# Performance work log

Measured on AMD Instinct MI355X. Metric: run time of the kernel, lower is better.

## Reference

```python
import jax, jax.numpy as jnp
import numpy as np

B, T, S, DM, H, HID = 4, 1024, 1024, 1024, 16, 4096
DEPTH = DM // H


def setup_inputs() -> dict:
    key = jax.random.key(0)
    ks = jax.random.split(key, 32)
    n = lambda k, shape, scale=1.0: jax.random.normal(k, shape, dtype=jnp.float32) * scale
    w_scale = 1.0 / np.sqrt(DM)
    inp = {
        "x": n(ks[0], (B, T, DM)),
        "enc_out": n(ks[1], (B, S, DM)),
        # causal mask: 1 where attention is forbidden (TF convention mask*-1e9)
        "look_ahead_mask": jnp.broadcast_to(
            jnp.triu(jnp.ones((T, T), jnp.float32), k=1), (B, 1, T, T)),
        "padding_mask": jnp.zeros((B, 1, 1, S), jnp.float32),
    }
    # self-attention MHA params
    names = ["wq1", "wk1", "wv1", "wo1", "wq2", "wk2", "wv2", "wo2"]
    for i, nm in enumerate(names):
        inp[nm] = n(ks[2 + i], (DM, DM), w_scale)
        inp["b" + nm[1:]] = jnp.zeros((DM,), jnp.float32)
    # FFN
    inp["wh"] = n(ks[10], (DM, HID), w_scale)
    inp["bh"] = jnp.zeros((HID,), jnp.float32)
    inp["wout"] = n(ks[11], (HID, DM), 1.0 / np.sqrt(HID))
    inp["bout"] = jnp.zeros((DM,), jnp.float32)
    for i in (1, 2, 3):
        inp[f"g{i}"] = jnp.ones((DM,), jnp.float32)
        inp[f"be{i}"] = jnp.zeros((DM,), jnp.float32)
    return inp


def _layer_norm(x, gamma, beta, eps=1e-6):
    mean = jnp.mean(x, axis=-1, keepdims=True)
    var = jnp.mean(jnp.square(x - mean), axis=-1, keepdims=True)
    return gamma * (x - mean) * jax.lax.rsqrt(var + eps) + beta


def _mha(q_in, k_in, v_in, mask, wq, bq, wk, bk, wv, bv, wo, bo):
    b = q_in.shape[0]
    split = lambda t: t.reshape(b, -1, H, DEPTH).transpose(0, 2, 1, 3)  # [b,h,s,d]
    Q = split(q_in @ wq + bq)
    K = split(k_in @ wk + bk)
    V = split(v_in @ wv + bv)
    scores = jnp.einsum("bhqd,bhkd->bhqk", Q, K) / jnp.sqrt(jnp.float32(DEPTH))
    scores = scores + mask * (-1e9)
    w = jax.nn.softmax(scores, axis=-1)
    out = jnp.einsum("bhqk,bhkd->bhqd", w, V)
    out = out.transpose(0, 2, 1, 3).reshape(b, -1, DM)
    return out @ wo + bo


def reference(x, enc_out, look_ahead_mask, padding_mask,
              wq1, bq1, wk1, bk1, wv1, bv1, wo1, bo1,
              wq2, bq2, wk2, bk2, wv2, bv2, wo2, bo2,
              wh, bh, wout, bout, g1, be1, g2, be2, g3, be3):
    # self-attention + residual + LN (dropout identity at inference)
    a1 = _mha(x, x, x, look_ahead_mask, wq1, bq1, wk1, bk1, wv1, bv1, wo1, bo1)
    h1 = _layer_norm(a1 + x, g1, be1)
    # cross-attention + residual + LN
    a2 = _mha(h1, enc_out, enc_out, padding_mask,
              wq2, bq2, wk2, bk2, wv2, bv2, wo2, bo2)
    h2 = _layer_norm(a2 + h1, g2, be2)
    # FFN + residual + LN
    f = jax.nn.relu(h2 @ wh + bh) @ wout + bout
    return _layer_norm(f + h2, g3, be3)
```

## Files before the change

kernel.cpp:

```cpp
#include <hip/hip_runtime.h>
#include <hip/hip_bf16.h>

typedef __bf16 bf16;
typedef __bf16 bf16x4 __attribute__((ext_vector_type(4)));
typedef __bf16 bf16x8 __attribute__((ext_vector_type(8)));
typedef float floatx4 __attribute__((ext_vector_type(4)));

#define MFMA16(a, b, c) __builtin_amdgcn_mfma_f32_16x16x32_bf16(a, b, c, 0, 0, 0)

#define BB   4
#define TT   1024
#define SS   1024
#define DMOD 1024
#define NH   16
#define DH   64
#define HID  4096
#define MTOT (BB * TT)

__device__ __forceinline__ float loadf(const bf16* p)  { return (float)*p; }
__device__ __forceinline__ float loadf(const float* p) { return *p; }

__device__ __forceinline__ void gll16(const bf16* g, bf16* l) {
    __builtin_amdgcn_global_load_lds(
        (const __attribute__((address_space(1))) void*)g,
        (__attribute__((address_space(3))) void*)l, 16, 0, 0);
}

__device__ __forceinline__ void xcd_swizzle2d(int& bx, int& by) {
    const int gx  = gridDim.x;
    const int nwg = gx * gridDim.y;
    const int lin = blockIdx.y * gx + blockIdx.x;
    const int q   = nwg >> 3;
    const int swz = (lin & 7) * q + (lin >> 3);
    bx = swz % gx;
    by = swz / gx;
}

struct TBatch { const float* src[8]; bf16* dst[8]; };

__global__ __launch_bounds__(256)
void transpose_sq_kernel(TBatch tb)
{
    __shared__ float t[64][65];
    const float* W = tb.src[blockIdx.z];
    bf16* WT = tb.dst[blockIdx.z];
    const int k0 = blockIdx.y * 64, n0 = blockIdx.x * 64;
    const int tid = threadIdx.x;
    const int r = tid >> 4, c = (tid & 15) * 4;
    #pragma unroll
    for (int i = 0; i < 4; ++i) {
        float4 v = *(const float4*)(W + (size_t)(k0 + i * 16 + r) * DMOD + n0 + c);
        t[i * 16 + r][c + 0] = v.x; t[i * 16 + r][c + 1] = v.y;
        t[i * 16 + r][c + 2] = v.z; t[i * 16 + r][c + 3] = v.w;
    }
    __syncthreads();
    #pragma unroll
    for (int i = 0; i < 4; ++i) {
        int n = i * 16 + r;
        bf16x4 o;
        #pragma unroll
        for (int j = 0; j < 4; ++j) o[j] = (bf16)t[c + j][n];
        *(bf16x4*)(WT + (size_t)(n0 + n) * DMOD + k0 + c) = o;
    }
}

__global__ __launch_bounds__(256)
void transpose_kernel(const float* __restrict__ W, bf16* __restrict__ WT, int K, int N)
{
    __shared__ float t[64][65];
    const int k0 = blockIdx.y * 64, n0 = blockIdx.x * 64;
    const int tid = threadIdx.x;
    const int r = tid >> 4, c = (tid & 15) * 4;
    #pragma unroll
    for (int i = 0; i < 4; ++i) {
        float4 v = *(const float4*)(W + (size_t)(k0 + i * 16 + r) * N + n0 + c);
        t[i * 16 + r][c + 0] = v.x; t[i * 16 + r][c + 1] = v.y;
        t[i * 16 + r][c + 2] = v.z; t[i * 16 + r][c + 3] = v.w;
    }
    __syncthreads();
    #pragma unroll
    for (int i = 0; i < 4; ++i) {
        int n = i * 16 + r;
        bf16x4 o;
        #pragma unroll
        for (int j = 0; j < 4; ++j) o[j] = (bf16)t[c + j][n];
        *(bf16x4*)(WT + (size_t)(n0 + n) * K + k0 + c) = o;
    }
}

__global__ __launch_bounds__(256)
void vtrans_kernel(const bf16* __restrict__ in, int ldi, bf16* __restrict__ out)
{
    __shared__ bf16 t[64][72];
    const int r0 = blockIdx.y * 64;
    const int c0 = blockIdx.x * 64;
    const int tid = threadIdx.x;
    const int rr = tid >> 3;
    const int c8 = (tid & 7) * 8;
    #pragma unroll
    for (int i = 0; i < 2; ++i) {
        int row = i * 32 + rr;
        bf16x8 v = *(const bf16x8*)(in + (size_t)(r0 + row) * ldi + c0 + c8);
        *(bf16x8*)(&t[row][c8]) = v;
    }
    __syncthreads();
    #pragma unroll
    for (int i = 0; i < 2; ++i) {
        int col = i * 32 + rr;
        bf16x8 v;
        #pragma unroll
        for (int j = 0; j < 8; ++j) v[j] = t[c8 + j][col];
        *(bf16x8*)(out + (size_t)(c0 + col) * MTOT + r0 + c8) = v;
    }
}

__global__ __launch_bounds__(256)
void cvt_kernel(const float* __restrict__ in, bf16* __restrict__ out, int n4)
{
    int i = blockIdx.x * 256 + threadIdx.x;
    if (i < n4) {
        float4 v = ((const float4*)in)[i];
        bf16x4 o = { (bf16)v.x, (bf16)v.y, (bf16)v.z, (bf16)v.w };
        ((bf16x4*)out)[i] = o;
    }
}

__global__ __launch_bounds__(256)
void bias_concat_kernel(const float* bq1, const float* bk1, const float* bv1,
                        const float* bk2, const float* bv2, float* __restrict__ biasc)
{
    int i = blockIdx.x * 256 + threadIdx.x;
    float v;
    if      (i < 1024) v = bq1[i];
    else if (i < 2048) v = bk1[i - 1024];
    else if (i < 3072) v = bv1[i - 2048];
    else if (i < 4096) v = bk2[i - 3072];
    else               v = bv2[i - 4096];
    if (i < 5120) biasc[i] = v;
}

template <int EPI, typename TR>
__global__ __launch_bounds__(256, 4)
void gemm128k32_kernel(const bf16* __restrict__ A, int lda, const bf16* __restrict__ B,
                       const float* __restrict__ bias, const TR* __restrict__ resid,
                       bf16* __restrict__ out, int M, int N, int K)
{
    __shared__ bf16 Al[2][128 * 32];
    __shared__ bf16 Bl[2][128 * 32];

    const int tid  = threadIdx.x;
    const int wave = tid >> 6;
    const int lane = tid & 63;
    const int l16  = lane & 15;
    const int quad = lane >> 4;
    int bx, by;
    xcd_swizzle2d(bx, by);
    const int bm   = by * 128;
    const int bn   = bx * 128;
    const int wm   = (wave >> 1) * 64;
    const int wn   = (wave & 1) * 64;
    const int lrow = lane >> 2;
    const int scol = ((lane & 3) ^ ((lane >> 3) & 3)) * 8;

    floatx4 acc[4][4] = {};
    const int ntk = K / 32;

    auto STAGE = [&](int kt, int buf) {
        const int k0 = kt * 32;
        #pragma unroll
        for (int i = 0; i < 2; ++i) {
            int r0 = (wave * 2 + i) * 16;
            gll16(A + (size_t)(bm + r0 + lrow) * lda + k0 + scol, &Al[buf][r0 * 32]);
            gll16(B + (size_t)(bn + r0 + lrow) * K   + k0 + scol, &Bl[buf][r0 * 32]);
        }
    };

    auto COMPUTE = [&](int buf) {
        bf16x8 af[4], bg[4];
        const int xo = ((quad ^ ((l16 >> 1) & 3))) * 8;
        #pragma unroll
        for (int mt = 0; mt < 4; ++mt)
            af[mt] = *(const bf16x8*)(&Al[buf][(wm + mt * 16 + l16) * 32 + xo]);
        #pragma unroll
        for (int nt = 0; nt < 4; ++nt)
            bg[nt] = *(const bf16x8*)(&Bl[buf][(wn + nt * 16 + l16) * 32 + xo]);
        #pragma unroll
        for (int mt = 0; mt < 4; ++mt)
            #pragma unroll
            for (int nt = 0; nt < 4; ++nt)
                acc[mt][nt] = MFMA16(af[mt], bg[nt], acc[mt][nt]);
    };

    STAGE(0, 0);
    asm volatile("s_waitcnt vmcnt(0)" ::: "memory");
    __builtin_amdgcn_s_barrier();

    int cur = 0;
    for (int t = 0; t < ntk - 1; ++t) {
        STAGE(t + 1, cur ^ 1);
        COMPUTE(cur);
        asm volatile("s_waitcnt vmcnt(0) lgkmcnt(0)" ::: "memory");
        __builtin_amdgcn_s_barrier();
        cur ^= 1;
    }
    COMPUTE(cur);

    #pragma unroll
    for (int mt = 0; mt < 4; ++mt) {
        int row0 = bm + wm + mt * 16 + quad * 4;
        #pragma unroll
        for (int nt = 0; nt < 4; ++nt) {
            int col = bn + wn + nt * 16 + l16;
            float bv = bias[col];
            #pragma unroll
            for (int r = 0; r < 4; ++r) {
                float v = acc[mt][nt][r] + bv;
                size_t idx = (size_t)(row0 + r) * N + col;
                if (EPI == 1) v = fmaxf(v, 0.0f);
                if (EPI == 2) v += loadf(resid + idx);
                out[idx] = (bf16)v;
            }
        }
    }
}

template <int EPI, typename TR>
__global__ __launch_bounds__(256, 4)
void gemm6464_kernel(const bf16* __restrict__ A, int lda, const bf16* __restrict__ B,
                     const float* __restrict__ bias, const TR* __restrict__ resid,
                     bf16* __restrict__ out, int M, int N, int K)
{
    __shared__ bf16 Al[2][64 * 64];
    __shared__ bf16 Bl[2][64 * 64];

    const int tid  = threadIdx.x;
    const int wave = tid >> 6;
    const int lane = tid & 63;
    const int l16  = lane & 15;
    const int quad = lane >> 4;
    int bx, by;
    xcd_swizzle2d(bx, by);
    const int bm   = by * 64;
    const int bn   = bx * 64;
    const int wm   = (wave >> 1) * 32;
    const int wn   = (wave & 1) * 32;
    const int lrow = lane >> 3;
    const int scol = ((lane & 7) ^ lrow) * 8;

    floatx4 acc[2][2] = {};
    const int ntk = K / 64;

    auto STAGE = [&](int kt, int buf) {
        const int k0 = kt * 64;
        #pragma unroll
        for (int i = 0; i < 2; ++i) {
            int r0 = wave * 16 + i * 8;
            gll16(A + (size_t)(bm + r0 + lrow) * lda + k0 + scol, &Al[buf][r0 * 64]);
            gll16(B + (size_t)(bn + r0 + lrow) * K   + k0 + scol, &Bl[buf][r0 * 64]);
        }
    };

    auto COMPUTE = [&](int buf) {
        #pragma unroll
        for (int ks = 0; ks < 2; ++ks) {
            bf16x8 af[2], bg[2];
            const int xo = ((ks * 4 + quad) ^ (l16 & 7)) * 8;
            #pragma unroll
            for (int mt = 0; mt < 2; ++mt)
                af[mt] = *(const bf16x8*)(&Al[buf][(wm + mt * 16 + l16) * 64 + xo]);
            #pragma unroll
            for (int nt = 0; nt < 2; ++nt)
                bg[nt] = *(const bf16x8*)(&Bl[buf][(wn + nt * 16 + l16) * 64 + xo]);
            #pragma unroll
            for (int mt = 0; mt < 2; ++mt)
                #pragma unroll
                for (int nt = 0; nt < 2; ++nt)
                    acc[mt][nt] = MFMA16(af[mt], bg[nt], acc[mt][nt]);
        }
    };

    STAGE(0, 0);
    asm volatile("s_waitcnt vmcnt(0)" ::: "memory");
    __builtin_amdgcn_s_barrier();

    int cur = 0;
    for (int t = 0; t < ntk - 1; ++t) {
        STAGE(t + 1, cur ^ 1);
        COMPUTE(cur);
        asm volatile("s_waitcnt vmcnt(0) lgkmcnt(0)" ::: "memory");
        __builtin_amdgcn_s_barrier();
        cur ^= 1;
    }
    COMPUTE(cur);

    #pragma unroll
    for (int mt = 0; mt < 2; ++mt) {
        int row0 = bm + wm + mt * 16 + quad * 4;
        #pragma unroll
        for (int nt = 0; nt < 2; ++nt) {
            int col = bn + wn + nt * 16 + l16;
            float bv = bias[col];
            #pragma unroll
            for (int r = 0; r < 4; ++r) {
                float v = acc[mt][nt][r] + bv;
                size_t idx = (size_t)(row0 + r) * N + col;
                if (EPI == 1) v = fmaxf(v, 0.0f);
                if (EPI == 2) v += loadf(resid + idx);
                out[idx] = (bf16)v;
            }
        }
    }
}

template <int CAUSAL>
__global__ __launch_bounds__(256, 3)
void attn_kernel(const bf16* __restrict__ Q, int ldq, const bf16* __restrict__ K, int ldk,
                 const bf16* __restrict__ Vt, bf16* __restrict__ O, int ldo)
{
    __shared__ bf16 Kl[2][64 * 64];
    __shared__ bf16 Vl[2][64 * 64];
    __shared__ bf16 Pl[4 * 16 * 72];

    const int tid  = threadIdx.x;
    const int wave = tid >> 6;
    const int lane = tid & 63;
    const int l16  = lane & 15;
    const int quad = lane >> 4;
    int bx, byy, bz;
    {
        const int lin = (blockIdx.z * 16 + blockIdx.y) * 16 + blockIdx.x;
        const int swz = (lin & 7) * 128 + (lin >> 3);
        bx  = swz & 15;
        byy = (swz >> 4) & 15;
        bz  = swz >> 8;
    }
    const int qb   = CAUSAL ? (15 - bx) : bx;
    const int h    = byy;
    const int b    = bz;

    const int qrow0 = b * TT + qb * 64 + wave * 16;
    const int colh  = h * DH;
    const int lr8   = lane >> 3;
    const int lc8s  = ((lane & 7) ^ lr8) * 8;

    bf16x8 qa[2];
    #pragma unroll
    for (int c = 0; c < 2; ++c)
        qa[c] = *(const bf16x8*)(Q + (size_t)(qrow0 + l16) * ldq + colh + c * 32 + quad * 8);

    floatx4 o[5] = {};
    const float C = 0.125f * 1.4426950408889634f;
    bf16x8 onesf;
    {
        bf16 ov = (bf16)((l16 == 0) ? 1.0f : 0.0f);
        #pragma unroll
        for (int j = 0; j < 8; ++j) onesf[j] = ov;
    }

    const int ntiles = CAUSAL ? qb + 1 : (SS / 64);
    bf16* pw = Pl + wave * (16 * 72);

    auto STAGE = [&](int t, int buf) {
        const int kv0 = t * 64;
        #pragma unroll
        for (int i = 0; i < 2; ++i) {
            int r0 = wave * 16 + i * 8;
            gll16(K  + (size_t)(b * SS + kv0 + r0 + lr8) * ldk + colh + lc8s, &Kl[buf][r0 * 64]);
            gll16(Vt + (size_t)(colh + r0 + lr8) * MTOT + b * SS + kv0 + lc8s, &Vl[buf][r0 * 64]);
        }
    };

    auto COMPUTE = [&](int t, int buf) {
        const int xo0 = (quad ^ (l16 & 7)) * 8;
        const int xo1 = ((4 + quad) ^ (l16 & 7)) * 8;

        floatx4 s[4];
        #pragma unroll
        for (int nt = 0; nt < 4; ++nt) {
            bf16x8 kb0 = *(const bf16x8*)(&Kl[buf][(nt * 16 + l16) * 64 + xo0]);
            bf16x8 kb1 = *(const bf16x8*)(&Kl[buf][(nt * 16 + l16) * 64 + xo1]);
            floatx4 z = {};
            z = MFMA16(qa[0], kb0, z);
            z = MFMA16(qa[1], kb1, z);
            s[nt] = z;
        }

        const bool dm = CAUSAL && (t == qb);
        #pragma unroll
        for (int nt = 0; nt < 4; ++nt)
            #pragma unroll
            for (int r = 0; r < 4; ++r) {
                float sv = s[nt][r] * C;
                if (dm) {
                    int qg  = wave * 16 + quad * 4 + r;
                    int kvg = nt * 16 + l16;
                    if (kvg > qg) sv = -1e30f;
                }
                float pv = exp2f(sv);
                pw[(quad * 4 + r) * 72 + nt * 16 + l16] = (bf16)pv;
            }

        bf16x8 pa0 = *(const bf16x8*)(pw + l16 * 72 + quad * 8);
        bf16x8 pa1 = *(const bf16x8*)(pw + l16 * 72 + 32 + quad * 8);
        #pragma unroll
        for (int dt = 0; dt < 4; ++dt) {
            bf16x8 vb0 = *(const bf16x8*)(&Vl[buf][(dt * 16 + l16) * 64 + xo0]);
            bf16x8 vb1 = *(const bf16x8*)(&Vl[buf][(dt * 16 + l16) * 64 + xo1]);
            o[dt] = MFMA16(pa0, vb0, o[dt]);
            o[dt] = MFMA16(pa1, vb1, o[dt]);
        }
        o[4] = MFMA16(pa0, onesf, o[4]);
        o[4] = MFMA16(pa1, onesf, o[4]);
    };

    STAGE(0, 0);
    asm volatile("s_waitcnt vmcnt(0)" ::: "memory");
    __builtin_amdgcn_s_barrier();

    int cur = 0;
    for (int t = 0; t < ntiles - 1; ++t) {
        STAGE(t + 1, cur ^ 1);
        COMPUTE(t, cur);
        asm volatile("s_waitcnt vmcnt(0) lgkmcnt(0)" ::: "memory");
        __builtin_amdgcn_s_barrier();
        cur ^= 1;
    }
    COMPUTE(ntiles - 1, cur);

    #pragma unroll
    for (int r = 0; r < 4; ++r) {
        float lr  = __shfl(o[4][r], (lane & 48));
        float inv = __builtin_amdgcn_rcpf(lr);
        #pragma unroll
        for (int dt = 0; dt < 4; ++dt) {
            float ov = o[dt][r] * inv;
            size_t idx = (size_t)(qrow0 + quad * 4 + r) * ldo + colh + dt * 16 + l16;
            O[idx] = (bf16)ov;
        }
    }
}

template <typename TO>
__global__ __launch_bounds__(256)
void ln_kernel(const bf16* __restrict__ in, const float* __restrict__ g,
               const float* __restrict__ be, TO* __restrict__ out)
{
    const int row = blockIdx.x;
    const int tid = threadIdx.x;
    bf16x4 xv = *(const bf16x4*)(in + (size_t)row * DMOD + tid * 4);
    float x0 = (float)xv[0], x1 = (float)xv[1], x2 = (float)xv[2], x3 = (float)xv[3];

    float s = x0 + x1 + x2 + x3;
    #pragma unroll
    for (int off = 32; off >= 1; off >>= 1) s += __shfl_xor(s, off);
    __shared__ float red1[4];
    __shared__ float red2[4];
    const int wave = tid >> 6;
    if ((tid & 63) == 0) red1[wave] = s;
    __syncthreads();
    float mean = (red1[0] + red1[1] + red1[2] + red1[3]) * (1.0f / DMOD);

    float d0 = x0 - mean, d1 = x1 - mean, d2 = x2 - mean, d3 = x3 - mean;
    float sq = d0 * d0 + d1 * d1 + d2 * d2 + d3 * d3;
    #pragma unroll
    for (int off = 32; off >= 1; off >>= 1) sq += __shfl_xor(sq, off);
    if ((tid & 63) == 0) red2[wave] = sq;
    __syncthreads();
    float var = (red2[0] + red2[1] + red2[2] + red2[3]) * (1.0f / DMOD);
    float rs = rsqrtf(var + 1e-6f);

    int c = tid * 4;
    size_t o0 = (size_t)row * DMOD + c;
    out[o0 + 0] = (TO)(g[c + 0] * d0 * rs + be[c + 0]);
    out[o0 + 1] = (TO)(g[c + 1] * d1 * rs + be[c + 1]);
    out[o0 + 2] = (TO)(g[c + 2] * d2 * rs + be[c + 2]);
    out[o0 + 3] = (TO)(g[c + 3] * d3 * rs + be[c + 3]);
}

extern "C" void kernel_launch(void* const* d_in, const int* in_sizes, int n_in,
                              void* d_out, int out_size, void* d_ws, size_t ws_size,
                              hipStream_t stream)
{
    const float* x   = (const float*)d_in[0];
    const float* enc = (const float*)d_in[1];
    const float* wq1 = (const float*)d_in[4];  const float* bq1 = (const float*)d_in[5];
    const float* wk1 = (const float*)d_in[6];  const float* bk1 = (const float*)d_in[7];
    const float* wv1 = (const float*)d_in[8];  const float* bv1 = (const float*)d_in[9];
    const float* wo1 = (const float*)d_in[10]; const float* bo1 = (const float*)d_in[11];
    const float* wq2 = (const float*)d_in[12]; const float* bq2 = (const float*)d_in[13];
    const float* wk2 = (const float*)d_in[14]; const float* bk2 = (const float*)d_in[15];
    const float* wv2 = (const float*)d_in[16]; const float* bv2 = (const float*)d_in[17];
    const float* wo2 = (const float*)d_in[18]; const float* bo2 = (const float*)d_in[19];
    const float* wh  = (const float*)d_in[20]; const float* bh  = (const float*)d_in[21];
    const float* wou = (const float*)d_in[22]; const float* bou = (const float*)d_in[23];
    const float* g1  = (const float*)d_in[24]; const float* be1 = (const float*)d_in[25];
    const float* g2  = (const float*)d_in[26]; const float* be2 = (const float*)d_in[27];
    const float* g3  = (const float*)d_in[28]; const float* be3 = (const float*)d_in[29];

    const int M = MTOT;
    const size_t MB = 1u << 20;
    dim3 blk(256);

    char* ws = (char*)d_ws;
    bf16*  WT    = (bf16*)(ws);
    float* biasc = (float*)(ws + 8 * MB);
    bf16*  xb    = (bf16*)(ws + 9 * MB);
    bf16*  h1    = (bf16*)(ws + 9 * MB);
    bf16*  tmpb3 = (bf16*)(ws + 9 * MB);
    bf16*  encb  = (bf16*)(ws + 17 * MB);
    bf16*  Vt2   = (bf16*)(ws + 17 * MB);
    bf16*  ffn   = (bf16*)(ws + 17 * MB);
    bf16*  qkv   = (bf16*)(ws + 25 * MB);
    bf16*  kvb   = qkv + (size_t)M * 1024;
    bf16*  tmpb2 = qkv + (size_t)M * 1024;
    bf16*  Vt1   = (bf16*)(ws + 49 * MB);
    bf16*  tmpb1 = (bf16*)(ws + 49 * MB);
    bf16*  h2    = (bf16*)(ws + 49 * MB);

    dim3 gThi(HID / 64, DMOD / 64);
    dim3 gTout(DMOD / 64, HID / 64);
    dim3 gVt(DMOD / 64, M / 64);
    dim3 gQKV(3072 / 128, M / 128);
    dim3 gKV(2048 / 128, M / 128);
    dim3 gH(HID / 128, M / 128);
    dim3 gN6464(DMOD / 64, M / 64);
    dim3 gA(TT / 64, NH, BB);
    const size_t W1M = (size_t)1024 * 1024;

    cvt_kernel<<<dim3(M * DMOD / 4 / 256), blk, 0, stream>>>(x, xb, M * DMOD / 4);
    cvt_kernel<<<dim3(M * DMOD / 4 / 256), blk, 0, stream>>>(enc, encb, M * DMOD / 4);
    bias_concat_kernel<<<dim3(20), blk, 0, stream>>>(bq1, bk1, bv1, bk2, bv2, biasc);

    {
        TBatch tb;
        tb.src[0] = wq1; tb.dst[0] = WT + 0 * W1M;
        tb.src[1] = wk1; tb.dst[1] = WT + 1 * W1M;
        tb.src[2] = wv1; tb.dst[2] = WT + 2 * W1M;
        tb.src[3] = wo1; tb.dst[3] = WT + 3 * W1M;
        tb.src[4] = tb.src[5] = tb.src[6] = tb.src[7] = wq1;
        tb.dst[4] = tb.dst[5] = tb.dst[6] = tb.dst[7] = WT;
        dim3 g4(16, 16, 4);
        transpose_sq_kernel<<<g4, blk, 0, stream>>>(tb);
    }

    gemm128k32_kernel<0, bf16><<<gQKV, blk, 0, stream>>>(xb, 1024, WT, biasc,
                                                         (const bf16*)nullptr, qkv, M, 3072, 1024);
    vtrans_kernel<<<gVt, blk, 0, stream>>>(qkv + 2048, 3072, Vt1);
    attn_kernel<1><<<gA, blk, 0, stream>>>(qkv, 3072, qkv + 1024, 3072, Vt1, qkv, 3072);
    gemm6464_kernel<2, float><<<gN6464, blk, 0, stream>>>(qkv, 3072, WT + 3 * W1M, bo1, x,
                                                          tmpb1, M, 1024, 1024);
    ln_kernel<bf16><<<dim3(M), blk, 0, stream>>>(tmpb1, g1, be1, h1);

    {
        TBatch tb;
        tb.src[0] = wq2; tb.dst[0] = WT + 0 * W1M;
        tb.src[1] = wk2; tb.dst[1] = WT + 1 * W1M;
        tb.src[2] = wv2; tb.dst[2] = WT + 2 * W1M;
        tb.src[3] = wo2; tb.dst[3] = WT + 3 * W1M;
        tb.src[4] = tb.src[5] = tb.src[6] = tb.src[7] = wq2;
        tb.dst[4] = tb.dst[5] = tb.dst[6] = tb.dst[7] = WT;
        dim3 g4(16, 16, 4);
        transpose_sq_kernel<<<g4, blk, 0, stream>>>(tb);
    }

    gemm6464_kernel<0, bf16><<<gN6464, blk, 0, stream>>>(h1, 1024, WT, bq2, (const bf16*)nullptr,
                                                         qkv, M, 1024, 1024);
    gemm128k32_kernel<0, bf16><<<gKV, blk, 0, stream>>>(encb, 1024, WT + 1 * W1M, biasc + 3072,
                                                        (const bf16*)nullptr, kvb, M, 2048, 1024);
    vtrans_kernel<<<gVt, blk, 0, stream>>>(kvb + 1024, 2048, Vt2);
    attn_kernel<0><<<gA, blk, 0, stream>>>(qkv, 1024, kvb, 2048, Vt2, qkv, 1024);
    gemm6464_kernel<2, bf16><<<gN6464, blk, 0, stream>>>(qkv, 1024, WT + 3 * W1M, bo2, h1,
                                                         tmpb2, M, 1024, 1024);
    ln_kernel<bf16><<<dim3(M), blk, 0, stream>>>(tmpb2, g2, be2, h2);

    transpose_kernel<<<gThi, blk, 0, stream>>>(wh, WT, DMOD, HID);
    gemm128k32_kernel<1, bf16><<<gH, blk, 0, stream>>>(h2, 1024, WT, bh, (const bf16*)nullptr,
                                                       ffn, M, HID, 1024);
    transpose_kernel<<<gTout, blk, 0, stream>>>(wou, WT, HID, DMOD);
    gemm6464_kernel<2, bf16><<<gN6464, blk, 0, stream>>>(ffn, 4096, WT, bou, h2,
                                                         tmpb3, M, 1024, 4096);
    ln_kernel<float><<<dim3(M), blk, 0, stream>>>(tmpb3, g3, be3, (float*)d_out);
}
```

Baseline: 500.9 us.

## Use 64x128 tiles for QKV/KV GEMMs and split-K FFN2 fused into LayerNorm

Adds a 64x128 tile GEMM with BK=32 for the fused QKV and cross-attention KV projections, which doubles the number of blocks and raises occupancy. Adds a split-K (K/2) 64x64 GEMM for the FFN down-projection. It writes two bf16 partials, which a new LayerNorm kernel sums together with the bias and residual. This spreads the K=4096 GEMM over more blocks, at the cost of extra partial-buffer traffic and bf16 rounding of the partials. The split-K path is taken only when the workspace is at least 66MB.

```diff
diff --git a/kernel.cpp b/kernel.cpp
--- a/kernel.cpp
+++ b/kernel.cpp
@@ -177,7 +177,7 @@
 
     auto COMPUTE = [&](int buf) {
         bf16x8 af[4], bg[4];
-        const int xo = ((quad ^ ((l16 >> 1) & 3))) * 8;
+        const int xo = (quad ^ ((l16 >> 1) & 3)) * 8;
         #pragma unroll
         for (int mt = 0; mt < 4; ++mt)
             af[mt] = *(const bf16x8*)(&Al[buf][(wm + mt * 16 + l16) * 32 + xo]);
@@ -219,6 +219,90 @@
                 if (EPI == 1) v = fmaxf(v, 0.0f);
                 if (EPI == 2) v += loadf(resid + idx);
                 out[idx] = (bf16)v;
+            }
+        }
+    }
+}
+
+__global__ __launch_bounds__(256, 6)
+void gemm64128k32_kernel(const bf16* __restrict__ A, int lda, const bf16* __restrict__ B,
+                         const float* __restrict__ bias, bf16* __restrict__ out,
+                         int M, int N, int K)
+{
+    __shared__ bf16 Al[2][64 * 32];
+    __shared__ bf16 Bl[2][128 * 32];
+
+    const int tid  = threadIdx.x;
+    const int wave = tid >> 6;
+    const int lane = tid & 63;
+    const int l16  = lane & 15;
+    const int quad = lane >> 4;
+    int bx, by;
+    xcd_swizzle2d(bx, by);
+    const int bm   = by * 64;
+    const int bn   = bx * 128;
+    const int wm   = (wave >> 1) * 32;
+    const int wn   = (wave & 1) * 64;
+    const int lrow = lane >> 2;
+    const int scol = ((lane & 3) ^ ((lane >> 3) & 3)) * 8;
+
+    floatx4 acc[2][4] = {};
+    const int ntk = K / 32;
+
+    auto STAGE = [&](int kt, int buf) {
+        const int k0 = kt * 32;
+        {
+            int r0 = wave * 16;
+            gll16(A + (size_t)(bm + r0 + lrow) * lda + k0 + scol, &Al[buf][r0 * 32]);
+        }
+        #pragma unroll
+        for (int i = 0; i < 2; ++i) {
+            int r0 = wave * 32 + i * 16;
+            gll16(B + (size_t)(bn + r0 + lrow) * K + k0 + scol, &Bl[buf][r0 * 32]);
+        }
+    };
+
+    auto COMPUTE = [&](int buf) {
+        bf16x8 af[2], bg[4];
+        const int xo = (quad ^ ((l16 >> 1) & 3)) * 8;
+        #pragma unroll
+        for (int mt = 0; mt < 2; ++mt)
+            af[mt] = *(const bf16x8*)(&Al[buf][(wm + mt * 16 + l16) * 32 + xo]);
+        #pragma unroll
+        for (int nt = 0; nt < 4; ++nt)
+            bg[nt] = *(const bf16x8*)(&Bl[buf][(wn + nt * 16 + l16) * 32 + xo]);
+        #pragma unroll
+        for (int mt = 0; mt < 2; ++mt)
+            #pragma unroll
+            for (int nt = 0; nt < 4; ++nt)
+                acc[mt][nt] = MFMA16(af[mt], bg[nt], acc[mt][nt]);
+    };
+
+    STAGE(0, 0);
+    asm volatile("s_waitcnt vmcnt(0)" ::: "memory");
+    __builtin_amdgcn_s_barrier();
+
+    int cur = 0;
+    for (int t = 0; t < ntk - 1; ++t) {
+        STAGE(t + 1, cur ^ 1);
+        COMPUTE(cur);
+        asm volatile("s_waitcnt vmcnt(0) lgkmcnt(0)" ::: "memory");
+        __builtin_amdgcn_s_barrier();
+        cur ^= 1;
+    }
+    COMPUTE(cur);
+
+    #pragma unroll
+    for (int mt = 0; mt < 2; ++mt) {
+        int row0 = bm + wm + mt * 16 + quad * 4;
+        #pragma unroll
+        for (int nt = 0; nt < 4; ++nt) {
+            int col = bn + wn + nt * 16 + l16;
+            float bv = bias[col];
+            #pragma unroll
+            for (int r = 0; r < 4; ++r) {
+                float v = acc[mt][nt][r] + bv;
+                out[(size_t)(row0 + r) * N + col] = (bf16)v;
             }
         }
     }
@@ -312,6 +396,84 @@
     }
 }
 
+__global__ __launch_bounds__(256, 8)
+void gemm6464k32s_kernel(const bf16* __restrict__ A, int lda, const bf16* __restrict__ B,
+                         bf16* __restrict__ p0, bf16* __restrict__ p1,
+                         int M, int N, int K)
+{
+    __shared__ bf16 Al[2][64 * 32];
+    __shared__ bf16 Bl[2][64 * 32];
+
+    const int tid  = threadIdx.x;
+    const int wave = tid >> 6;
+    const int lane = tid & 63;
+    const int l16  = lane & 15;
+    const int quad = lane >> 4;
+    int bx, by;
+    xcd_swizzle2d(bx, by);
+    const int bm   = by * 64;
+    const int bn   = bx * 64;
+    const int wm   = (wave >> 1) * 32;
+    const int wn   = (wave & 1) * 32;
+    const int lrow = lane >> 2;
+    const int scol = ((lane & 3) ^ ((lane >> 3) & 3)) * 8;
+    const int kh    = K >> 1;
+    const int kbase = blockIdx.z * kh;
+    bf16* outp = blockIdx.z ? p1 : p0;
+
+    floatx4 acc[2][2] = {};
+    const int ntk = kh / 32;
+
+    auto STAGE = [&](int kt, int buf) {
+        const int k0 = kbase + kt * 32;
+        int r0 = wave * 16;
+        gll16(A + (size_t)(bm + r0 + lrow) * lda + k0 + scol, &Al[buf][r0 * 32]);
+        gll16(B + (size_t)(bn + r0 + lrow) * K   + k0 + scol, &Bl[buf][r0 * 32]);
+    };
+
+    auto COMPUTE = [&](int buf) {
+        bf16x8 af[2], bg[2];
+        const int xo = (quad ^ ((l16 >> 1) & 3)) * 8;
+        #pragma unroll
+        for (int mt = 0; mt < 2; ++mt)
+            af[mt] = *(const bf16x8*)(&Al[buf][(wm + mt * 16 + l16) * 32 + xo]);
+        #pragma unroll
+        for (int nt = 0; nt < 2; ++nt)
+            bg[nt] = *(const bf16x8*)(&Bl[buf][(wn + nt * 16 + l16) * 32 + xo]);
+        #pragma unroll
+        for (int mt = 0; mt < 2; ++mt)
+            #pragma unroll
+            for (int nt = 0; nt < 2; ++nt)
+                acc[mt][nt] = MFMA16(af[mt], bg[nt], acc[mt][nt]);
+    };
+
+    STAGE(0, 0);
+    asm volatile("s_waitcnt vmcnt(0)" ::: "memory");
+    __builtin_amdgcn_s_barrier();
+
+    int cur = 0;
+    for (int t = 0; t < ntk - 1; ++t) {
+        STAGE(t + 1, cur ^ 1);
+        COMPUTE(cur);
+        asm volatile("s_waitcnt vmcnt(0) lgkmcnt(0)" ::: "memory");
+        __builtin_amdgcn_s_barrier();
+        cur ^= 1;
+    }
+    COMPUTE(cur);
+
+    #pragma unroll
+    for (int mt = 0; mt < 2; ++mt) {
+        int row0 = bm + wm + mt * 16 + quad * 4;
+        #pragma unroll
+        for (int nt = 0; nt < 2; ++nt) {
+            int col = bn + wn + nt * 16 + l16;
+            #pragma unroll
+            for (int r = 0; r < 4; ++r)
+                outp[(size_t)(row0 + r) * N + col] = (bf16)acc[mt][nt][r];
+        }
+    }
+}
+
 template <int CAUSAL>
 __global__ __launch_bounds__(256, 3)
 void attn_kernel(const bf16* __restrict__ Q, int ldq, const bf16* __restrict__ K, int ldk,
@@ -475,6 +637,50 @@
     out[o0 + 1] = (TO)(g[c + 1] * d1 * rs + be[c + 1]);
     out[o0 + 2] = (TO)(g[c + 2] * d2 * rs + be[c + 2]);
     out[o0 + 3] = (TO)(g[c + 3] * d3 * rs + be[c + 3]);
+}
+
+__global__ __launch_bounds__(256)
+void ln_sum_kernel(const bf16* __restrict__ p0, const bf16* __restrict__ p1,
+                   const float* __restrict__ bias, const bf16* __restrict__ resid,
+                   const float* __restrict__ g, const float* __restrict__ be,
+                   float* __restrict__ out)
+{
+    const int row = blockIdx.x;
+    const int tid = threadIdx.x;
+    const int c = tid * 4;
+    size_t i0 = (size_t)row * DMOD + c;
+    bf16x4 a = *(const bf16x4*)(p0 + i0);
+    bf16x4 b = *(const bf16x4*)(p1 + i0);
+    bf16x4 rr = *(const bf16x4*)(resid + i0);
+    float x0 = (float)a[0] + (float)b[0] + bias[c + 0] + (float)rr[0];
+    float x1 = (float)a[1] + (float)b[1] + bias[c + 1] + (float)rr[1];
+    float x2 = (float)a[2] + (float)b[2] + bias[c + 2] + (float)rr[2];
+    float x3 = (float)a[3] + (float)b[3] + bias[c + 3] + (float)rr[3];
+
+    float s = x0 + x1 + x2 + x3;
+    #pragma unroll
+    for (int off = 32; off >= 1; off >>= 1) s += __shfl_xor(s, off);
+    __shared__ float red1[4];
+    __shared__ float red2[4];
+    const int wave = tid >> 6;
+    if ((tid & 63) == 0) red1[wave] = s;
+    __syncthreads();
+    float mean = (red1[0] + red1[1] + red1[2] + red1[3]) * (1.0f / DMOD);
+
+    float d0 = x0 - mean, d1 = x1 - mean, d2 = x2 - mean, d3 = x3 - mean;
+    float sq = d0 * d0 + d1 * d1 + d2 * d2 + d3 * d3;
+    #pragma unroll
+    for (int off = 32; off >= 1; off >>= 1) sq += __shfl_xor(sq, off);
+    if ((tid & 63) == 0) red2[wave] = sq;
+    __syncthreads();
+    float var = (red2[0] + red2[1] + red2[2] + red2[3]) * (1.0f / DMOD);
+    float rs = rsqrtf(var + 1e-6f);
+
+    size_t o0 = (size_t)row * DMOD + c;
+    out[o0 + 0] = g[c + 0] * d0 * rs + be[c + 0];
+    out[o0 + 1] = g[c + 1] * d1 * rs + be[c + 1];
+    out[o0 + 2] = g[c + 2] * d2 * rs + be[c + 2];
+    out[o0 + 3] = g[c + 3] * d3 * rs + be[c + 3];
 }
 
 extern "C" void kernel_launch(void* const* d_in, const int* in_sizes, int n_in,
@@ -507,6 +713,7 @@
     bf16*  xb    = (bf16*)(ws + 9 * MB);
     bf16*  h1    = (bf16*)(ws + 9 * MB);
     bf16*  tmpb3 = (bf16*)(ws + 9 * MB);
+    bf16*  p0    = (bf16*)(ws + 9 * MB);
     bf16*  encb  = (bf16*)(ws + 17 * MB);
     bf16*  Vt2   = (bf16*)(ws + 17 * MB);
     bf16*  ffn   = (bf16*)(ws + 17 * MB);
@@ -516,14 +723,17 @@
     bf16*  Vt1   = (bf16*)(ws + 49 * MB);
     bf16*  tmpb1 = (bf16*)(ws + 49 * MB);
     bf16*  h2    = (bf16*)(ws + 49 * MB);
+    bf16*  p1    = (bf16*)(ws + 57 * MB);
+    const bool splitk = (ws_size >= (66ull << 20));
 
     dim3 gThi(HID / 64, DMOD / 64);
     dim3 gTout(DMOD / 64, HID / 64);
     dim3 gVt(DMOD / 64, M / 64);
-    dim3 gQKV(3072 / 128, M / 128);
-    dim3 gKV(2048 / 128, M / 128);
+    dim3 gQKV(3072 / 128, M / 64);
+    dim3 gKV(2048 / 128, M / 64);
     dim3 gH(HID / 128, M / 128);
     dim3 gN6464(DMOD / 64, M / 64);
+    dim3 gFFN2s(DMOD / 64, M / 64, 2);
     dim3 gA(TT / 64, NH, BB);
     const size_t W1M = (size_t)1024 * 1024;
 
@@ -543,8 +753,7 @@
         transpose_sq_kernel<<<g4, blk, 0, stream>>>(tb);
     }
 
-    gemm128k32_kernel<0, bf16><<<gQKV, blk, 0, stream>>>(xb, 1024, WT, biasc,
-                                                         (const bf16*)nullptr, qkv, M, 3072, 1024);
+    gemm64128k32_kernel<<<gQKV, blk, 0, stream>>>(xb, 1024, WT, biasc, qkv, M, 3072, 1024);
     vtrans_kernel<<<gVt, blk, 0, stream>>>(qkv + 2048, 3072, Vt1);
     attn_kernel<1><<<gA, blk, 0, stream>>>(qkv, 3072, qkv + 1024, 3072, Vt1, qkv, 3072);
     gemm6464_kernel<2, float><<<gN6464, blk, 0, stream>>>(qkv, 3072, WT + 3 * W1M, bo1, x,
@@ -565,8 +774,8 @@
 
     gemm6464_kernel<0, bf16><<<gN6464, blk, 0, stream>>>(h1, 1024, WT, bq2, (const bf16*)nullptr,
                                                          qkv, M, 1024, 1024);
-    gemm128k32_kernel<0, bf16><<<gKV, blk, 0, stream>>>(encb, 1024, WT + 1 * W1M, biasc + 3072,
-                                                        (const bf16*)nullptr, kvb, M, 2048, 1024);
+    gemm64128k32_kernel<<<gKV, blk, 0, stream>>>(encb, 1024, WT + 1 * W1M, biasc + 3072,
+                                                 kvb, M, 2048, 1024);
     vtrans_kernel<<<gVt, blk, 0, stream>>>(kvb + 1024, 2048, Vt2);
     attn_kernel<0><<<gA, blk, 0, stream>>>(qkv, 1024, kvb, 2048, Vt2, qkv, 1024);
     gemm6464_kernel<2, bf16><<<gN6464, blk, 0, stream>>>(qkv, 1024, WT + 3 * W1M, bo2, h1,
@@ -577,7 +786,12 @@
     gemm128k32_kernel<1, bf16><<<gH, blk, 0, stream>>>(h2, 1024, WT, bh, (const bf16*)nullptr,
                                                        ffn, M, HID, 1024);
     transpose_kernel<<<gTout, blk, 0, stream>>>(wou, WT, HID, DMOD);
-    gemm6464_kernel<2, bf16><<<gN6464, blk, 0, stream>>>(ffn, 4096, WT, bou, h2,
-                                                         tmpb3, M, 1024, 4096);
-    ln_kernel<float><<<dim3(M), blk, 0, stream>>>(tmpb3, g3, be3, (float*)d_out);
-}
+    if (splitk) {
+        gemm6464k32s_kernel<<<gFFN2s, blk, 0, stream>>>(ffn, 4096, WT, p0, p1, M, 1024, 4096);
+        ln_sum_kernel<<<dim3(M), blk, 0, stream>>>(p0, p1, bou, h2, g3, be3, (float*)d_out);
+    } else {
+        gemm6464_kernel<2, bf16><<<gN6464, blk, 0, stream>>>(ffn, 4096, WT, bou, h2,
+                                                             tmpb3, M, 1024, 4096);
+        ln_kernel<float><<<dim3(M), blk, 0, stream>>>(tmpb3, g3, be3, (float*)d_out);
+    }
+}
```

New measurement: 539.1 us. 1.08x slower.

## Load attention K/V directly from global memory instead of LDS staging

Applied to the files above, without the earlier changes.

The attention kernel no longer stages K and V tiles into double-buffered shared memory. Each wave now reads its MFMA operands straight from global memory, relying on L1/L2 caching. This removes the block barriers and about 32KB of LDS per block, and the occupancy hint is raised from 3 to 4 blocks per SM. The cost is that each of the four waves now issues its own global loads for the same K/V tiles, with no prefetch overlap, so load latency is exposed unless occupancy hides it.

```diff
diff --git a/kernel.cpp b/kernel.cpp
--- a/kernel.cpp
+++ b/kernel.cpp
@@ -177,7 +177,7 @@
 
     auto COMPUTE = [&](int buf) {
         bf16x8 af[4], bg[4];
-        const int xo = ((quad ^ ((l16 >> 1) & 3))) * 8;
+        const int xo = (quad ^ ((l16 >> 1) & 3)) * 8;
         #pragma unroll
         for (int mt = 0; mt < 4; ++mt)
             af[mt] = *(const bf16x8*)(&Al[buf][(wm + mt * 16 + l16) * 32 + xo]);
@@ -313,12 +313,10 @@
 }
 
 template <int CAUSAL>
-__global__ __launch_bounds__(256, 3)
+__global__ __launch_bounds__(256, 4)
 void attn_kernel(const bf16* __restrict__ Q, int ldq, const bf16* __restrict__ K, int ldk,
                  const bf16* __restrict__ Vt, bf16* __restrict__ O, int ldo)
 {
-    __shared__ bf16 Kl[2][64 * 64];
-    __shared__ bf16 Vl[2][64 * 64];
     __shared__ bf16 Pl[4 * 16 * 72];
 
     const int tid  = threadIdx.x;
@@ -340,8 +338,6 @@
 
     const int qrow0 = b * TT + qb * 64 + wave * 16;
     const int colh  = h * DH;
-    const int lr8   = lane >> 3;
-    const int lc8s  = ((lane & 7) ^ lr8) * 8;
 
     bf16x8 qa[2];
     #pragma unroll
@@ -360,25 +356,15 @@
     const int ntiles = CAUSAL ? qb + 1 : (SS / 64);
     bf16* pw = Pl + wave * (16 * 72);
 
-    auto STAGE = [&](int t, int buf) {
+    for (int t = 0; t < ntiles; ++t) {
         const int kv0 = t * 64;
-        #pragma unroll
-        for (int i = 0; i < 2; ++i) {
-            int r0 = wave * 16 + i * 8;
-            gll16(K  + (size_t)(b * SS + kv0 + r0 + lr8) * ldk + colh + lc8s, &Kl[buf][r0 * 64]);
-            gll16(Vt + (size_t)(colh + r0 + lr8) * MTOT + b * SS + kv0 + lc8s, &Vl[buf][r0 * 64]);
-        }
-    };
-
-    auto COMPUTE = [&](int t, int buf) {
-        const int xo0 = (quad ^ (l16 & 7)) * 8;
-        const int xo1 = ((4 + quad) ^ (l16 & 7)) * 8;
 
         floatx4 s[4];
         #pragma unroll
         for (int nt = 0; nt < 4; ++nt) {
-            bf16x8 kb0 = *(const bf16x8*)(&Kl[buf][(nt * 16 + l16) * 64 + xo0]);
-            bf16x8 kb1 = *(const bf16x8*)(&Kl[buf][(nt * 16 + l16) * 64 + xo1]);
+            const bf16* kp = K + (size_t)(b * SS + kv0 + nt * 16 + l16) * ldk + colh + quad * 8;
+            bf16x8 kb0 = *(const bf16x8*)(kp);
+            bf16x8 kb1 = *(const bf16x8*)(kp + 32);
             floatx4 z = {};
             z = MFMA16(qa[0], kb0, z);
             z = MFMA16(qa[1], kb1, z);
@@ -404,28 +390,15 @@
         bf16x8 pa1 = *(const bf16x8*)(pw + l16 * 72 + 32 + quad * 8);
         #pragma unroll
         for (int dt = 0; dt < 4; ++dt) {
-            bf16x8 vb0 = *(const bf16x8*)(&Vl[buf][(dt * 16 + l16) * 64 + xo0]);
-            bf16x8 vb1 = *(const bf16x8*)(&Vl[buf][(dt * 16 + l16) * 64 + xo1]);
+            const bf16* vp = Vt + (size_t)(colh + dt * 16 + l16) * MTOT + b * SS + kv0 + quad * 8;
+            bf16x8 vb0 = *(const bf16x8*)(vp);
+            bf16x8 vb1 = *(const bf16x8*)(vp + 32);
             o[dt] = MFMA16(pa0, vb0, o[dt]);
             o[dt] = MFMA16(pa1, vb1, o[dt]);
         }
         o[4] = MFMA16(pa0, onesf, o[4]);
         o[4] = MFMA16(pa1, onesf, o[4]);
-    };
-
-    STAGE(0, 0);
-    asm volatile("s_waitcnt vmcnt(0)" ::: "memory");
-    __builtin_amdgcn_s_barrier();
-
-    int cur = 0;
-    for (int t = 0; t < ntiles - 1; ++t) {
-        STAGE(t + 1, cur ^ 1);
-        COMPUTE(t, cur);
-        asm volatile("s_waitcnt vmcnt(0) lgkmcnt(0)" ::: "memory");
-        __builtin_amdgcn_s_barrier();
-        cur ^= 1;
-    }
-    COMPUTE(ntiles - 1, cur);
+    }
 
     #pragma unroll
     for (int r = 0; r < 4; ++r) {
```

Result: slower. 659.2 us (+31.6%).
